# Performance work log

Measured on AMD Instinct MI355X. Metric: run time of the kernel, lower is better.

## Reference

```python
import jax, jax.numpy as jnp
import numpy as np

HEADS = 8
DIM_HEAD = 64
SCALE = DIM_HEAD ** -0.5


def setup_inputs() -> dict:
    key = jax.random.key(0)
    ks = jax.random.split(key, 5)
    B, N, M, D = 8, 1024, 1024, 512
    inner = HEADS * DIM_HEAD  # 512
    return {
        "x": jax.random.normal(ks[0], (B, N, D), dtype=jnp.float32),
        "context": jax.random.normal(ks[1], (B, M, D), dtype=jnp.float32),
        "Wq": jax.random.normal(ks[2], (D, inner), dtype=jnp.float32) * (D ** -0.5),
        "Wkv": jax.random.normal(ks[3], (D, 2 * inner), dtype=jnp.float32) * (D ** -0.5),
        "Wo": jax.random.normal(ks[4], (inner, D), dtype=jnp.float32) * (inner ** -0.5),
        "bo": jnp.zeros((D,), dtype=jnp.float32),
    }


def reference(x, context, Wq, Wkv, Wo, bo):
    B, N, D = x.shape
    M = context.shape[1]
    q = x @ Wq                      # [B, N, inner]
    kv = context @ Wkv              # [B, M, 2*inner]
    k, v = jnp.split(kv, 2, axis=-1)
    # b n (h d) -> b h n d
    split_heads = lambda t: t.reshape(t.shape[0], t.shape[1], HEADS, DIM_HEAD).transpose(0, 2, 1, 3)
    q, k, v = split_heads(q), split_heads(k), split_heads(v)
    dots = jnp.einsum('bhid,bhjd->bhij', q, k) * SCALE  # [B, H, N, M]
    attn = jax.nn.softmax(dots, axis=-1)
    out = jnp.einsum('bhij,bhjd->bhid', attn, v)        # [B, H, N, d]
    out = out.transpose(0, 2, 1, 3).reshape(B, N, HEADS * DIM_HEAD)
    return out @ Wo + bo            # [B, N, D]
```

## Files before the change

kernel.cpp:

```cpp
#include <hip/hip_runtime.h>
#include <stdint.h>

#define LOG2E 1.44269504088896340736f
#define QSCALE (0.125f * LOG2E)

typedef __bf16 bf16x8 __attribute__((ext_vector_type(8)));
typedef float floatx4 __attribute__((ext_vector_type(4)));

__device__ __forceinline__ unsigned short bfbits(float f) {
  __bf16 h = (__bf16)f;
  return __builtin_bit_cast(unsigned short, h);
}

__device__ __forceinline__ float fast_exp2(float x) {
#if __has_builtin(__builtin_amdgcn_exp2f)
  return __builtin_amdgcn_exp2f(x);
#else
  return exp2f(x);
#endif
}

__device__ __forceinline__ void gl2lds16(const void* g, void* l) {
  __builtin_amdgcn_global_load_lds((const __attribute__((address_space(1))) void*)g,
                                   (__attribute__((address_space(3))) void*)l, 16, 0, 0);
}

__global__ __launch_bounds__(256)
void prep_kernel(const float* __restrict__ x, const float* __restrict__ ctx,
                 const float* __restrict__ Wq, const float* __restrict__ Wkv,
                 const float* __restrict__ Wo,
                 unsigned short* __restrict__ Xb, unsigned short* __restrict__ Cb,
                 unsigned short* __restrict__ WqT, unsigned short* __restrict__ WkvT,
                 unsigned short* __restrict__ WoT) {
  int blk = blockIdx.x;
  int tid = threadIdx.x;
  if (blk < 8192) {
    const float* in = blk < 4096 ? x : ctx;
    unsigned short* out = blk < 4096 ? Xb : Cb;
    int i = (((blk & 4095) * 256) + tid) * 4;
    float4 v = *(const float4*)(in + i);
    unsigned long long pk = (unsigned long long)bfbits(v.x)
                          | ((unsigned long long)bfbits(v.y) << 16)
                          | ((unsigned long long)bfbits(v.z) << 32)
                          | ((unsigned long long)bfbits(v.w) << 48);
    *(unsigned long long*)(out + i) = pk;
  } else {
    __shared__ float tile[32][33];
    int t = blk - 8192;
    const float* in; unsigned short* out; int N; int tb;
    if (t < 256)      { in = Wq;  out = WqT;  N = 512;  tb = t; }
    else if (t < 768) { in = Wkv; out = WkvT; N = 1024; tb = t - 256; }
    else              { in = Wo;  out = WoT;  N = 512;  tb = t - 768; }
    const int K = 512;
    int nbx = N / 32;
    int n0 = (tb % nbx) * 32, k0 = (tb / nbx) * 32;
    int tx = tid & 31, ty = tid >> 5;
#pragma unroll
    for (int r = ty; r < 32; r += 8)
      tile[r][tx] = in[(long)(k0 + r) * N + n0 + tx];
    __syncthreads();
#pragma unroll
    for (int r = ty; r < 32; r += 8)
      out[(long)(n0 + r) * K + k0 + tx] = bfbits(tile[tx][r]);
  }
}

__global__ __launch_bounds__(256)
void proj_gemm(const unsigned short* __restrict__ Xb, const unsigned short* __restrict__ Cb,
               const unsigned short* __restrict__ WqT, const unsigned short* __restrict__ WkvT,
               unsigned short* __restrict__ Qb, unsigned short* __restrict__ Kb,
               unsigned short* __restrict__ Vt) {
  __shared__ unsigned short As[128 * 32];
  __shared__ unsigned short Bs[128 * 32];

  int idx = blockIdx.x;
  const unsigned short* A; const unsigned short* Bt;
  long bm, bn; int role;
  if (idx < 256) { role = 0; A = Xb; Bt = WqT;  bn = (long)(idx & 3) * 128; bm = (long)(idx >> 2) * 128; }
  else { idx -= 256; role = 1; A = Cb; Bt = WkvT; bn = (long)(idx & 7) * 128; bm = (long)(idx >> 3) * 128; }

  const int tid = threadIdx.x;
  const int wave = tid >> 6;
  const int lane = tid & 63;
  const int l15 = lane & 15;
  const int q4 = lane >> 4;
  const int wm = (wave & 1) * 64;
  const int wn = (wave >> 1) * 64;
  const int K = 512;

  floatx4 acc[4][4];
#pragma unroll
  for (int i = 0; i < 4; ++i)
#pragma unroll
    for (int j = 0; j < 4; ++j) { acc[i][j][0]=0.f; acc[i][j][1]=0.f; acc[i][j][2]=0.f; acc[i][j][3]=0.f; }

  for (int k0 = 0; k0 < K; k0 += 32) {
#pragma unroll
    for (int cc = 0; cc < 2; ++cc) {
      int c = cc * 256 + tid;
      int r = c >> 2, kc = c & 3;
      gl2lds16(A + (bm + r) * (long)K + k0 + kc * 8, (char*)As + c * 16);
      gl2lds16(Bt + (bn + r) * (long)K + k0 + kc * 8, (char*)Bs + c * 16);
    }
    __syncthreads();
    bf16x8 af[4], bfr[4];
#pragma unroll
    for (int i = 0; i < 4; ++i)
      af[i] = *(const bf16x8*)(As + (wm + i * 16 + l15) * 32 + q4 * 8);
#pragma unroll
    for (int j = 0; j < 4; ++j)
      bfr[j] = *(const bf16x8*)(Bs + (wn + j * 16 + l15) * 32 + q4 * 8);
#pragma unroll
    for (int i = 0; i < 4; ++i)
#pragma unroll
      for (int j = 0; j < 4; ++j)
        acc[i][j] = __builtin_amdgcn_mfma_f32_16x16x32_bf16(af[i], bfr[j], acc[i][j], 0, 0, 0);
    __syncthreads();
  }

  const bool vrole = (role == 1) && (bn >= 512);
#pragma unroll
  for (int i = 0; i < 4; ++i) {
#pragma unroll
    for (int j = 0; j < 4; ++j) {
      long col = bn + wn + j * 16 + l15;
      if (vrole) {
        long h = (col - 512) >> 6, d = col & 63;
        long row0 = bm + wm + i * 16 + q4 * 4;
        long b = row0 >> 10, m0 = row0 & 1023;
        unsigned long long pk = (unsigned long long)bfbits(acc[i][j][0])
                              | ((unsigned long long)bfbits(acc[i][j][1]) << 16)
                              | ((unsigned long long)bfbits(acc[i][j][2]) << 32)
                              | ((unsigned long long)bfbits(acc[i][j][3]) << 48);
        *(unsigned long long*)(Vt + ((b * 8 + h) * 64 + d) * 1024 + m0) = pk;
      } else {
        long h = col >> 6, d = col & 63;
#pragma unroll
        for (int r = 0; r < 4; ++r) {
          long row = bm + wm + i * 16 + q4 * 4 + r;
          long b = row >> 10, n = row & 1023;
          float v = acc[i][j][r];
          if (role == 0) Qb[((b * 8 + h) * 1024 + n) * 64 + d] = bfbits(v * QSCALE);
          else           Kb[((b * 8 + h) * 1024 + n) * 64 + d] = bfbits(v);
        }
      }
    }
  }
}

__global__ __launch_bounds__(256)
void attn_kernel(const unsigned short* __restrict__ Qb,
                 const unsigned short* __restrict__ Kb,
                 const unsigned short* __restrict__ Vt,
                 unsigned short* __restrict__ Ob)
{
  __shared__ unsigned short Ksm[2][4096];
  __shared__ unsigned short Vsm[2][4096];
  __shared__ unsigned short Psm[128 * 64];

  const int tid = threadIdx.x;
  const int wave = tid >> 6;
  const int lane = tid & 63;
  const int l15 = lane & 15;
  const int q4 = lane >> 4;
  const int bh = blockIdx.x;
  const int nb = blockIdx.y;

  const long qrow0 = (long)bh * 1024 + nb * 128 + wave * 32;

  bf16x8 qf[2][2];
#pragma unroll
  for (int qn = 0; qn < 2; ++qn)
#pragma unroll
    for (int ks = 0; ks < 2; ++ks)
      qf[qn][ks] = *(const bf16x8*)(Qb + (qrow0 + qn * 16 + l15) * 64 + ks * 32 + q4 * 8);

  floatx4 acc[2][4];
#pragma unroll
  for (int i = 0; i < 2; ++i)
#pragma unroll
    for (int d = 0; d < 4; ++d) { acc[i][d][0]=0.f; acc[i][d][1]=0.f; acc[i][d][2]=0.f; acc[i][d][3]=0.f; }
  float suml[2] = {0.0f, 0.0f};

  const unsigned short* Kbase = Kb + (long)bh * 65536;
  const unsigned short* Vbase = Vt + (long)bh * 65536;
  int koff[2], voff[2], lds16[2];
#pragma unroll
  for (int cc = 0; cc < 2; ++cc) {
    int c = cc * 256 + tid;
    int jrow = c >> 3;
    int cact = (c & 7) ^ (jrow & 7);
    koff[cc] = jrow * 64 + cact * 8;
    voff[cc] = jrow * 1024 + cact * 8;
    lds16[cc] = c * 16;
  }

  const int s7 = l15 & 7;
  int kfo[2][4];
  int pao[2][2];
  int pwo[2][4];
#pragma unroll
  for (int ks = 0; ks < 2; ++ks) {
#pragma unroll
    for (int jn = 0; jn < 4; ++jn)
      kfo[ks][jn] = (jn * 16 + l15) * 64 + (((ks * 4 + q4) ^ s7) * 8);
#pragma unroll
    for (int i = 0; i < 2; ++i)
      pao[ks][i] = (wave * 32 + i * 16 + l15) * 64 + (((ks * 4 + q4) ^ s7) * 8);
  }
#pragma unroll
  for (int qn = 0; qn < 2; ++qn)
#pragma unroll
    for (int jn = 0; jn < 4; ++jn)
      pwo[qn][jn] = (wave * 32 + qn * 16 + l15) * 64 + (((jn * 2 + (q4 >> 1)) ^ s7) * 8) + (q4 & 1) * 4;

#pragma unroll
  for (int cc = 0; cc < 2; ++cc) {
    gl2lds16(Kbase + koff[cc], (char*)Ksm[0] + lds16[cc]);
    gl2lds16(Vbase + voff[cc], (char*)Vsm[0] + lds16[cc]);
  }

#define ATTN_TILE(TIDX, CUR, STAGE)                                                          \
  {                                                                                          \
    __syncthreads();                                                                         \
    if (STAGE) {                                                                             \
      _Pragma("unroll")                                                                      \
      for (int cc = 0; cc < 2; ++cc) {                                                       \
        gl2lds16(Kbase + ((TIDX) + 1) * 4096 + koff[cc], (char*)Ksm[(CUR) ^ 1] + lds16[cc]); \
        gl2lds16(Vbase + ((TIDX) + 1) * 64 + voff[cc], (char*)Vsm[(CUR) ^ 1] + lds16[cc]);   \
      }                                                                                      \
    }                                                                                        \
    floatx4 st[4][2];                                                                        \
    _Pragma("unroll")                                                                        \
    for (int jn = 0; jn < 4; ++jn)                                                           \
      _Pragma("unroll")                                                                      \
      for (int qn = 0; qn < 2; ++qn) {                                                       \
        st[jn][qn][0] = 0.f; st[jn][qn][1] = 0.f; st[jn][qn][2] = 0.f; st[jn][qn][3] = 0.f;  \
      }                                                                                      \
    _Pragma("unroll")                                                                        \
    for (int ks = 0; ks < 2; ++ks) {                                                         \
      bf16x8 kfr[4];                                                                         \
      _Pragma("unroll")                                                                      \
      for (int jn = 0; jn < 4; ++jn)                                                         \
        kfr[jn] = *(const bf16x8*)(Ksm[(CUR)] + kfo[ks][jn]);                                \
      _Pragma("unroll")                                                                      \
      for (int jn = 0; jn < 4; ++jn)                                                         \
        _Pragma("unroll")                                                                    \
        for (int qn = 0; qn < 2; ++qn)                                                       \
          st[jn][qn] = __builtin_amdgcn_mfma_f32_16x16x32_bf16(kfr[jn], qf[qn][ks],          \
                                                               st[jn][qn], 0, 0, 0);         \
    }                                                                                        \
    _Pragma("unroll")                                                                        \
    for (int qn = 0; qn < 2; ++qn) {                                                         \
      _Pragma("unroll")                                                                      \
      for (int jn = 0; jn < 4; ++jn) {                                                       \
        float p0 = fast_exp2(st[jn][qn][0]);                                                 \
        float p1 = fast_exp2(st[jn][qn][1]);                                                 \
        float p2 = fast_exp2(st[jn][qn][2]);                                                 \
        float p3 = fast_exp2(st[jn][qn][3]);                                                 \
        suml[qn] += (p0 + p1) + (p2 + p3);                                                   \
        unsigned int lo = (unsigned int)bfbits(p0) | ((unsigned int)bfbits(p1) << 16);       \
        unsigned int hi = (unsigned int)bfbits(p2) | ((unsigned int)bfbits(p3) << 16);       \
        unsigned long long pk = (unsigned long long)lo | ((unsigned long long)hi << 32);     \
        *(unsigned long long*)(Psm + pwo[qn][jn]) = pk;                                      \
      }                                                                                      \
    }                                                                                        \
    __asm__ volatile("s_waitcnt lgkmcnt(0)" ::: "memory");                                   \
    _Pragma("unroll")                                                                        \
    for (int ks = 0; ks < 2; ++ks) {                                                         \
      bf16x8 pa[2], vb[4];                                                                   \
      _Pragma("unroll")                                                                      \
      for (int i = 0; i < 2; ++i)                                                            \
        pa[i] = *(const bf16x8*)(Psm + pao[ks][i]);                                          \
      _Pragma("unroll")                                                                      \
      for (int dn = 0; dn < 4; ++dn)                                                         \
        vb[dn] = *(const bf16x8*)(Vsm[(CUR)] + kfo[ks][dn]);                                 \
      _Pragma("unroll")                                                                      \
      for (int i = 0; i < 2; ++i)                                                            \
        _Pragma("unroll")                                                                    \
        for (int dn = 0; dn < 4; ++dn)                                                       \
          acc[i][dn] = __builtin_amdgcn_mfma_f32_16x16x32_bf16(pa[i], vb[dn],                \
                                                               acc[i][dn], 0, 0, 0);         \
    }                                                                                        \
  }

  for (int tt = 0; tt < 8; ++tt) {
    ATTN_TILE(2 * tt, 0, true);
    ATTN_TILE(2 * tt + 1, 1, (tt < 7));
  }
#undef ATTN_TILE

  float inv[2], invr[2][4];
#pragma unroll
  for (int qn = 0; qn < 2; ++qn) {
    float l = suml[qn];
    l += __shfl_xor(l, 16, 64);
    l += __shfl_xor(l, 32, 64);
    inv[qn] = 1.0f / l;
#pragma unroll
    for (int r = 0; r < 4; ++r) invr[qn][r] = __shfl(inv[qn], q4 * 4 + r, 64);
  }

  const int b = bh >> 3, h = bh & 7;
#pragma unroll
  for (int i = 0; i < 2; ++i) {
#pragma unroll
    for (int dn = 0; dn < 4; ++dn) {
#pragma unroll
      for (int r = 0; r < 4; ++r) {
        long row = (long)b * 1024 + nb * 128 + wave * 32 + i * 16 + q4 * 4 + r;
        long col = h * 64 + dn * 16 + l15;
        Ob[row * 512 + col] = bfbits(acc[i][dn][r] * invr[i][r]);
      }
    }
  }
}

__global__ __launch_bounds__(256)
void out_gemm(const unsigned short* __restrict__ A,
              const unsigned short* __restrict__ Bt,
              float* __restrict__ outF, const float* __restrict__ bias) {
  __shared__ unsigned short As[64 * 32];
  __shared__ unsigned short Bs[128 * 32];

  const int tid = threadIdx.x;
  const int wave = tid >> 6;
  const int lane = tid & 63;
  const int l15 = lane & 15;
  const int q4 = lane >> 4;
  const int wm = (wave & 1) * 32;
  const int wn = (wave >> 1) * 64;
  const long bm = (long)blockIdx.y * 64;
  const long bn = (long)blockIdx.x * 128;
  const int K = 512, N = 512;

  floatx4 acc[2][4];
#pragma unroll
  for (int i = 0; i < 2; ++i)
#pragma unroll
    for (int j = 0; j < 4; ++j) { acc[i][j][0]=0.f; acc[i][j][1]=0.f; acc[i][j][2]=0.f; acc[i][j][3]=0.f; }

  for (int k0 = 0; k0 < K; k0 += 32) {
    {
      int r = tid >> 2, kc = tid & 3;
      gl2lds16(A + (bm + r) * (long)K + k0 + kc * 8, (char*)As + tid * 16);
    }
#pragma unroll
    for (int cc = 0; cc < 2; ++cc) {
      int c = cc * 256 + tid;
      int r = c >> 2, kc = c & 3;
      gl2lds16(Bt + (bn + r) * (long)K + k0 + kc * 8, (char*)Bs + c * 16);
    }
    __syncthreads();
    bf16x8 af[2], bfr[4];
#pragma unroll
    for (int i = 0; i < 2; ++i)
      af[i] = *(const bf16x8*)(As + (wm + i * 16 + l15) * 32 + q4 * 8);
#pragma unroll
    for (int j = 0; j < 4; ++j)
      bfr[j] = *(const bf16x8*)(Bs + (wn + j * 16 + l15) * 32 + q4 * 8);
#pragma unroll
    for (int i = 0; i < 2; ++i)
#pragma unroll
      for (int j = 0; j < 4; ++j)
        acc[i][j] = __builtin_amdgcn_mfma_f32_16x16x32_bf16(af[i], bfr[j], acc[i][j], 0, 0, 0);
    __syncthreads();
  }

#pragma unroll
  for (int i = 0; i < 2; ++i) {
#pragma unroll
    for (int j = 0; j < 4; ++j) {
      long col = bn + wn + j * 16 + l15;
      float bv = bias[col];
#pragma unroll
      for (int r = 0; r < 4; ++r) {
        long row = bm + wm + i * 16 + q4 * 4 + r;
        outF[row * (long)N + col] = acc[i][j][r] + bv;
      }
    }
  }
}

extern "C" void kernel_launch(void* const* d_in, const int* in_sizes, int n_in,
                              void* d_out, int out_size, void* d_ws, size_t ws_size,
                              hipStream_t stream) {
  const float* x   = (const float*)d_in[0];
  const float* ctx = (const float*)d_in[1];
  const float* Wq  = (const float*)d_in[2];
  const float* Wkv = (const float*)d_in[3];
  const float* Wo  = (const float*)d_in[4];
  const float* bo  = (const float*)d_in[5];
  float* out = (float*)d_out;

  char* ws = (char*)d_ws;
  unsigned short* Xb   = (unsigned short*)(ws);
  unsigned short* Cb   = (unsigned short*)(ws + (8u  << 20));
  unsigned short* WqT  = (unsigned short*)(ws + (16u << 20));
  unsigned short* WkvT = (unsigned short*)(ws + (17u << 20));
  unsigned short* WoT  = (unsigned short*)(ws + (19u << 20));
  unsigned short* Qb   = (unsigned short*)(ws + (20u << 20));
  unsigned short* Kb   = (unsigned short*)(ws + (28u << 20));
  unsigned short* Vt   = (unsigned short*)(ws + (36u << 20));
  unsigned short* Ob   = (unsigned short*)(ws + (44u << 20));

  prep_kernel<<<9216, 256, 0, stream>>>(x, ctx, Wq, Wkv, Wo, Xb, Cb, WqT, WkvT, WoT);
  proj_gemm<<<768, 256, 0, stream>>>(Xb, Cb, WqT, WkvT, Qb, Kb, Vt);
  attn_kernel<<<dim3(64, 8), 256, 0, stream>>>(Qb, Kb, Vt, Ob);
  out_gemm<<<dim3(4, 128), 256, 0, stream>>>(Ob, WoT, out, bo);
}
```

Baseline: 153.1 us.

## Widen GEMM K-tiles with XOR-swizzled LDS, remap blocks, prioritize MFMA in attention

Both projection GEMMs now stage 64-wide K tiles per iteration, halving the barrier count. The LDS layout is XOR-swizzled to avoid bank conflicts, and global-to-LDS offsets are precomputed once. Block indices are remapped across XCDs for better L2 locality, so out_gemm switches to a 1D grid. In the attention kernel, V fragment LDS reads are hoisted ahead of the softmax exp, and s_setprio is raised around the MFMA clusters. The exchange is higher register and LDS use, which may lower occupancy.

```diff
diff --git a/kernel.cpp b/kernel.cpp
--- a/kernel.cpp
+++ b/kernel.cpp
@@ -70,51 +70,71 @@
                const unsigned short* __restrict__ WqT, const unsigned short* __restrict__ WkvT,
                unsigned short* __restrict__ Qb, unsigned short* __restrict__ Kb,
                unsigned short* __restrict__ Vt) {
-  __shared__ unsigned short As[128 * 32];
-  __shared__ unsigned short Bs[128 * 32];
-
-  int idx = blockIdx.x;
+  __shared__ unsigned short As[128 * 64];
+  __shared__ unsigned short Bs[128 * 64];
+
+  int idx0 = blockIdx.x;
+  int idx = (idx0 & 7) * 96 + (idx0 >> 3);
   const unsigned short* A; const unsigned short* Bt;
   long bm, bn; int role;
   if (idx < 256) { role = 0; A = Xb; Bt = WqT;  bn = (long)(idx & 3) * 128; bm = (long)(idx >> 2) * 128; }
-  else { idx -= 256; role = 1; A = Cb; Bt = WkvT; bn = (long)(idx & 7) * 128; bm = (long)(idx >> 3) * 128; }
+  else { int j = idx - 256; role = 1; A = Cb; Bt = WkvT; bn = (long)(j & 7) * 128; bm = (long)(j >> 3) * 128; }
 
   const int tid = threadIdx.x;
   const int wave = tid >> 6;
   const int lane = tid & 63;
   const int l15 = lane & 15;
   const int q4 = lane >> 4;
+  const int s7 = l15 & 7;
   const int wm = (wave & 1) * 64;
   const int wn = (wave >> 1) * 64;
   const int K = 512;
 
+  int aoff[4], boff[4], lds16[4];
+#pragma unroll
+  for (int cc = 0; cc < 4; ++cc) {
+    int c = cc * 256 + tid;
+    int r = c >> 3, kc = c & 7;
+    int sw = (kc ^ (r & 7)) * 8;
+    aoff[cc] = (int)(bm + r) * K + sw;
+    boff[cc] = (int)(bn + r) * K + sw;
+    lds16[cc] = c * 16;
+  }
+  int arow[4], brow[4], csw[2];
+#pragma unroll
+  for (int i = 0; i < 4; ++i) {
+    arow[i] = (wm + i * 16 + l15) * 64;
+    brow[i] = (wn + i * 16 + l15) * 64;
+  }
+#pragma unroll
+  for (int ks = 0; ks < 2; ++ks) csw[ks] = ((ks * 4 + q4) ^ s7) * 8;
+
   floatx4 acc[4][4];
 #pragma unroll
   for (int i = 0; i < 4; ++i)
 #pragma unroll
     for (int j = 0; j < 4; ++j) { acc[i][j][0]=0.f; acc[i][j][1]=0.f; acc[i][j][2]=0.f; acc[i][j][3]=0.f; }
 
-  for (int k0 = 0; k0 < K; k0 += 32) {
-#pragma unroll
-    for (int cc = 0; cc < 2; ++cc) {
-      int c = cc * 256 + tid;
-      int r = c >> 2, kc = c & 3;
-      gl2lds16(A + (bm + r) * (long)K + k0 + kc * 8, (char*)As + c * 16);
-      gl2lds16(Bt + (bn + r) * (long)K + k0 + kc * 8, (char*)Bs + c * 16);
+  for (int k0 = 0; k0 < K; k0 += 64) {
+#pragma unroll
+    for (int cc = 0; cc < 4; ++cc) {
+      gl2lds16(A + aoff[cc] + k0, (char*)As + lds16[cc]);
+      gl2lds16(Bt + boff[cc] + k0, (char*)Bs + lds16[cc]);
     }
     __syncthreads();
-    bf16x8 af[4], bfr[4];
-#pragma unroll
-    for (int i = 0; i < 4; ++i)
-      af[i] = *(const bf16x8*)(As + (wm + i * 16 + l15) * 32 + q4 * 8);
-#pragma unroll
-    for (int j = 0; j < 4; ++j)
-      bfr[j] = *(const bf16x8*)(Bs + (wn + j * 16 + l15) * 32 + q4 * 8);
-#pragma unroll
-    for (int i = 0; i < 4; ++i)
-#pragma unroll
-      for (int j = 0; j < 4; ++j)
-        acc[i][j] = __builtin_amdgcn_mfma_f32_16x16x32_bf16(af[i], bfr[j], acc[i][j], 0, 0, 0);
+#pragma unroll
+    for (int ks = 0; ks < 2; ++ks) {
+      bf16x8 af[4], bfr[4];
+#pragma unroll
+      for (int i = 0; i < 4; ++i) af[i] = *(const bf16x8*)(As + arow[i] + csw[ks]);
+#pragma unroll
+      for (int j = 0; j < 4; ++j) bfr[j] = *(const bf16x8*)(Bs + brow[j] + csw[ks]);
+#pragma unroll
+      for (int i = 0; i < 4; ++i)
+#pragma unroll
+        for (int j = 0; j < 4; ++j)
+          acc[i][j] = __builtin_amdgcn_mfma_f32_16x16x32_bf16(af[i], bfr[j], acc[i][j], 0, 0, 0);
+    }
     __syncthreads();
   }
 
@@ -243,13 +263,21 @@
       _Pragma("unroll")                                                                      \
       for (int jn = 0; jn < 4; ++jn)                                                         \
         kfr[jn] = *(const bf16x8*)(Ksm[(CUR)] + kfo[ks][jn]);                                \
+      __builtin_amdgcn_s_setprio(1);                                                         \
       _Pragma("unroll")                                                                      \
       for (int jn = 0; jn < 4; ++jn)                                                         \
         _Pragma("unroll")                                                                    \
         for (int qn = 0; qn < 2; ++qn)                                                       \
           st[jn][qn] = __builtin_amdgcn_mfma_f32_16x16x32_bf16(kfr[jn], qf[qn][ks],          \
                                                                st[jn][qn], 0, 0, 0);         \
+      __builtin_amdgcn_s_setprio(0);                                                         \
     }                                                                                        \
+    bf16x8 vbt[2][4];        \
+    _Pragma("unroll")                                                                        \
+    for (int ks = 0; ks < 2; ++ks)                                                           \
+      _Pragma("unroll")                                                                      \
+      for (int dn = 0; dn < 4; ++dn)                                                         \
+        vbt[ks][dn] = *(const bf16x8*)(Vsm[(CUR)] + kfo[ks][dn]);                            \
     _Pragma("unroll")                                                                        \
     for (int qn = 0; qn < 2; ++qn) {                                                         \
       _Pragma("unroll")                                                                      \
@@ -268,19 +296,18 @@
     __asm__ volatile("s_waitcnt lgkmcnt(0)" ::: "memory");                                   \
     _Pragma("unroll")                                                                        \
     for (int ks = 0; ks < 2; ++ks) {                                                         \
-      bf16x8 pa[2], vb[4];                                                                   \
+      bf16x8 pa[2];                                                                          \
       _Pragma("unroll")                                                                      \
       for (int i = 0; i < 2; ++i)                                                            \
         pa[i] = *(const bf16x8*)(Psm + pao[ks][i]);                                          \
-      _Pragma("unroll")                                                                      \
-      for (int dn = 0; dn < 4; ++dn)                                                         \
-        vb[dn] = *(const bf16x8*)(Vsm[(CUR)] + kfo[ks][dn]);                                 \
+      __builtin_amdgcn_s_setprio(1);                                                         \
       _Pragma("unroll")                                                                      \
       for (int i = 0; i < 2; ++i)                                                            \
         _Pragma("unroll")                                                                    \
         for (int dn = 0; dn < 4; ++dn)                                                       \
-          acc[i][dn] = __builtin_amdgcn_mfma_f32_16x16x32_bf16(pa[i], vb[dn],                \
+          acc[i][dn] = __builtin_amdgcn_mfma_f32_16x16x32_bf16(pa[i], vbt[ks][dn],           \
                                                                acc[i][dn], 0, 0, 0);         \
+      __builtin_amdgcn_s_setprio(0);                                                         \
     }                                                                                        \
   }
 
@@ -320,50 +347,74 @@
 void out_gemm(const unsigned short* __restrict__ A,
               const unsigned short* __restrict__ Bt,
               float* __restrict__ outF, const float* __restrict__ bias) {
-  __shared__ unsigned short As[64 * 32];
-  __shared__ unsigned short Bs[128 * 32];
+  __shared__ unsigned short As[64 * 64];
+  __shared__ unsigned short Bs[128 * 64];
+
+  int bid = blockIdx.x;
+  int swz = (bid & 7) * 64 + (bid >> 3);
+  const long bm = (long)(swz >> 2) * 64;
+  const long bn = (long)(swz & 3) * 128;
 
   const int tid = threadIdx.x;
   const int wave = tid >> 6;
   const int lane = tid & 63;
   const int l15 = lane & 15;
   const int q4 = lane >> 4;
+  const int s7 = l15 & 7;
   const int wm = (wave & 1) * 32;
   const int wn = (wave >> 1) * 64;
-  const long bm = (long)blockIdx.y * 64;
-  const long bn = (long)blockIdx.x * 128;
   const int K = 512, N = 512;
 
+  int aoff[2], boff[4], alds[2], blds[4];
+#pragma unroll
+  for (int cc = 0; cc < 2; ++cc) {
+    int c = cc * 256 + tid;
+    int r = c >> 3, kc = c & 7;
+    aoff[cc] = (int)(bm + r) * K + (kc ^ (r & 7)) * 8;
+    alds[cc] = c * 16;
+  }
+#pragma unroll
+  for (int cc = 0; cc < 4; ++cc) {
+    int c = cc * 256 + tid;
+    int r = c >> 3, kc = c & 7;
+    boff[cc] = (int)(bn + r) * K + (kc ^ (r & 7)) * 8;
+    blds[cc] = c * 16;
+  }
+  int arow[2], brow[4], csw[2];
+#pragma unroll
+  for (int i = 0; i < 2; ++i) arow[i] = (wm + i * 16 + l15) * 64;
+#pragma unroll
+  for (int j = 0; j < 4; ++j) brow[j] = (wn + j * 16 + l15) * 64;
+#pragma unroll
+  for (int ks = 0; ks < 2; ++ks) csw[ks] = ((ks * 4 + q4) ^ s7) * 8;
+
   floatx4 acc[2][4];
 #pragma unroll
   for (int i = 0; i < 2; ++i)
 #pragma unroll
     for (int j = 0; j < 4; ++j) { acc[i][j][0]=0.f; acc[i][j][1]=0.f; acc[i][j][2]=0.f; acc[i][j][3]=0.f; }
 
-  for (int k0 = 0; k0 < K; k0 += 32) {
-    {
-      int r = tid >> 2, kc = tid & 3;
-      gl2lds16(A + (bm + r) * (long)K + k0 + kc * 8, (char*)As + tid * 16);
-    }
-#pragma unroll
-    for (int cc = 0; cc < 2; ++cc) {
-      int c = cc * 256 + tid;
-      int r = c >> 2, kc = c & 3;
-      gl2lds16(Bt + (bn + r) * (long)K + k0 + kc * 8, (char*)Bs + c * 16);
-    }
+  for (int k0 = 0; k0 < K; k0 += 64) {
+#pragma unroll
+    for (int cc = 0; cc < 2; ++cc)
+      gl2lds16(A + aoff[cc] + k0, (char*)As + alds[cc]);
+#pragma unroll
+    for (int cc = 0; cc < 4; ++cc)
+      gl2lds16(Bt + boff[cc] + k0, (char*)Bs + blds[cc]);
     __syncthreads();
-    bf16x8 af[2], bfr[4];
-#pragma unroll
-    for (int i = 0; i < 2; ++i)
-      af[i] = *(const bf16x8*)(As + (wm + i * 16 + l15) * 32 + q4 * 8);
-#pragma unroll
-    for (int j = 0; j < 4; ++j)
-      bfr[j] = *(const bf16x8*)(Bs + (wn + j * 16 + l15) * 32 + q4 * 8);
-#pragma unroll
-    for (int i = 0; i < 2; ++i)
-#pragma unroll
-      for (int j = 0; j < 4; ++j)
-        acc[i][j] = __builtin_amdgcn_mfma_f32_16x16x32_bf16(af[i], bfr[j], acc[i][j], 0, 0, 0);
+#pragma unroll
+    for (int ks = 0; ks < 2; ++ks) {
+      bf16x8 af[2], bfr[4];
+#pragma unroll
+      for (int i = 0; i < 2; ++i) af[i] = *(const bf16x8*)(As + arow[i] + csw[ks]);
+#pragma unroll
+      for (int j = 0; j < 4; ++j) bfr[j] = *(const bf16x8*)(Bs + brow[j] + csw[ks]);
+#pragma unroll
+      for (int i = 0; i < 2; ++i)
+#pragma unroll
+        for (int j = 0; j < 4; ++j)
+          acc[i][j] = __builtin_amdgcn_mfma_f32_16x16x32_bf16(af[i], bfr[j], acc[i][j], 0, 0, 0);
+    }
     __syncthreads();
   }
 
@@ -407,5 +458,5 @@
   prep_kernel<<<9216, 256, 0, stream>>>(x, ctx, Wq, Wkv, Wo, Xb, Cb, WqT, WkvT, WoT);
   proj_gemm<<<768, 256, 0, stream>>>(Xb, Cb, WqT, WkvT, Qb, Kb, Vt);
   attn_kernel<<<dim3(64, 8), 256, 0, stream>>>(Qb, Kb, Vt, Ob);
-  out_gemm<<<dim3(4, 128), 256, 0, stream>>>(Ob, WoT, out, bo);
-}
+  out_gemm<<<512, 256, 0, stream>>>(Ob, WoT, out, bo);
+}
```

After: 155.1 us. Within noise of the previous version (+1.3%).
